# Kernel tuning notes

Measured on AMD Instinct MI355X. Metric: run time of the kernel, lower is better.

Reference implementation:

```python
import jax, jax.numpy as jnp
import numpy as np

E = 200      # word2vec_embed_size
D = 768      # hidden_size
LN_EPS = 1e-12


def setup_inputs() -> dict:
    key = jax.random.key(0)
    ks = jax.random.split(key, 9)
    B, L, W = 16, 512, 8
    std = 0.02
    return {
        "word_embeddings": jax.random.normal(ks[0], (B, L, W, E), jnp.float32),
        "layer_output": jax.random.normal(ks[1], (B, L, D), jnp.float32),
        "Wt": jax.random.normal(ks[2], (D, E), jnp.float32) * std,   # word_transform weight
        "bt": jnp.zeros((D,), jnp.float32),
        "Ww": jax.random.normal(ks[3], (D, D), jnp.float32) * std,   # word_word_weight weight
        "bw": jnp.zeros((D,), jnp.float32),
        "attn_W": jax.random.normal(ks[4], (D, D), jnp.float32) * std,
        "ln_gamma": jnp.ones((D,), jnp.float32),
        "ln_beta": jnp.zeros((D,), jnp.float32),
    }


def _layernorm(x, gamma, beta):
    mu = jnp.mean(x, axis=-1, keepdims=True)
    var = jnp.mean(jnp.square(x - mu), axis=-1, keepdims=True)
    return (x - mu) * jax.lax.rsqrt(var + LN_EPS) * gamma + beta


def reference(word_embeddings, layer_output, Wt, bt, Ww, bw, attn_W, ln_gamma, ln_beta):
    # word_transform -> tanh -> word_word_weight   (dropout = identity in eval)
    wo = jnp.tanh(jnp.einsum('blwe,de->blwd', word_embeddings, Wt) + bt)
    wo = jnp.einsum('blwd,ed->blwe', wo, Ww) + bw          # [B,L,W,D]
    # bilinear char-word attention: (layer @ attn_W) . wo over D
    q = jnp.einsum('bld,de->ble', layer_output, attn_W)    # [B,L,D]
    alpha = jnp.einsum('bld,blwd->blw', q, wo)             # [B,L,W]
    alpha = jax.nn.softmax(alpha, axis=-1)
    weighted = jnp.einsum('blw,blwd->bld', alpha, wo)      # [B,L,D]
    fused = layer_output + weighted                        # residual (dropout = identity)
    return _layernorm(fused, ln_gamma, ln_beta)
```

## Files before the change

### kernel.cpp

```cpp
#include <hip/hip_runtime.h>
#include <hip/hip_bf16.h>


typedef __bf16 bf16_t;
typedef bf16_t bf16x4 __attribute__((ext_vector_type(4)));
typedef bf16_t bf16x8 __attribute__((ext_vector_type(8)));
typedef float f32x4 __attribute__((ext_vector_type(4)));

__device__ __forceinline__ bf16x4 cvt4(float4 v) {
  bf16x4 o;
  o[0] = (bf16_t)v.x; o[1] = (bf16_t)v.y;
  o[2] = (bf16_t)v.z; o[3] = (bf16_t)v.w;
  return o;
}
__device__ __forceinline__ bf16x8 cvt8(float4 a, float4 b) {
  bf16x8 v;
  v[0] = (bf16_t)a.x; v[1] = (bf16_t)a.y; v[2] = (bf16_t)a.z; v[3] = (bf16_t)a.w;
  v[4] = (bf16_t)b.x; v[5] = (bf16_t)b.y; v[6] = (bf16_t)b.z; v[7] = (bf16_t)b.w;
  return v;
}

__global__ void prep_all(const float* __restrict__ LO,
                         const float* __restrict__ Wt,
                         const float* __restrict__ Ww,
                         bf16_t* __restrict__ LOb, bf16_t* __restrict__ Wtb,
                         bf16_t* __restrict__ Wwf) {
  const int bid = blockIdx.x;
  if (bid >= 372) {
    const long u = (long)(bid - 372) * 256 + threadIdx.x;
    float4 a = *(const float4*)(LO + u * 8);
    float4 b = *(const float4*)(LO + u * 8 + 4);
    *(bf16x8*)&LOb[u * 8] = cvt8(a, b);
  } else if (bid < 84) {
    const int u = bid * 256 + threadIdx.x;
    const int lane = u & 63;
    const int v = u >> 6;
    const int kt = v % 7;
    const int v2 = v / 7;
    const int jg = v2 & 7, nt = v2 >> 3;
    const int l16 = lane & 15, quad = lane >> 4;
    const int n = nt * 128 + jg * 16 + l16;
    const int k0 = kt * 32 + quad * 8;
    float4 a = {0.f, 0.f, 0.f, 0.f}, b = {0.f, 0.f, 0.f, 0.f};
    if (k0 < 200) {
      a = *(const float4*)(Wt + n * 200 + k0);
      b = *(const float4*)(Wt + n * 200 + k0 + 4);
    }
    *(bf16x4*)&Wtb[u * 8] = cvt4(a);
    *(bf16x4*)&Wtb[u * 8 + 4] = cvt4(b);
  } else {
    const int u = (bid - 84) * 256 + threadIdx.x;
    const int lane = u & 63;
    const int v = u >> 6;
    const int kt = v % 24;
    const int jg = v / 24;
    const int l16 = lane & 15, quad = lane >> 4;
    const long n = jg * 16 + l16;
    const int k0 = kt * 32 + quad * 8;
    float4 a = *(const float4*)(Ww + n * 768 + k0);
    float4 b = *(const float4*)(Ww + n * 768 + k0 + 4);
    *(bf16x4*)&Wwf[u * 8] = cvt4(a);
    *(bf16x4*)&Wwf[u * 8 + 4] = cvt4(b);
  }
}

__global__ void prep_wc(const float* __restrict__ Wc, bf16_t* __restrict__ Wcf) {
  const int u = blockIdx.x * 256 + threadIdx.x;
  const int lane = u & 63;
  const int v = u >> 6;
  const int kt = v % 24;
  const int jg = v / 24;
  const int l16 = lane & 15, quad = lane >> 4;
  const int n = jg * 16 + l16;
  const int k0 = kt * 32 + quad * 8;
  bf16x8 o;
#pragma unroll
  for (int e = 0; e < 8; ++e) o[e] = (bf16_t)Wc[(long)(k0 + e) * 768 + n];
  *(bf16x8*)&Wcf[u * 8] = o;
}

__global__ __launch_bounds__(256, 2) void gemm_nn64(
    const float* __restrict__ A, const float* __restrict__ B,
    float* __restrict__ C) {
  __shared__ __align__(16) bf16_t As[64 * 32];
  __shared__ __align__(16) bf16_t Bs[32 * 64];

  const int t = threadIdx.x;
  const int lane = t & 63, wave = t >> 6;
  const int wr = wave >> 1, wc = wave & 1;
  const int quad = lane >> 4, l16 = lane & 15;
  const int m0 = blockIdx.y * 64, n0 = blockIdx.x * 64;

  f32x4 acc[2][2] = {};

  for (int kt = 0; kt < 24; ++kt) {
    const int k0 = kt * 32;
#pragma unroll
    for (int r = 0; r < 2; ++r) {
      const int f = r * 256 + t;
      const int arow = f >> 3, ak = (f & 7) * 4;
      *(bf16x4*)&As[arow * 32 + ak] =
          cvt4(*(const float4*)(A + (m0 + arow) * 768 + k0 + ak));
      const int brow = f >> 4, bc = (f & 15) * 4;
      *(bf16x4*)&Bs[brow * 64 + bc] =
          cvt4(*(const float4*)(B + (long)(k0 + brow) * 768 + n0 + bc));
    }
    __syncthreads();
    bf16x8 af[2], bfv[2];
#pragma unroll
    for (int i = 0; i < 2; ++i)
      af[i] = *(const bf16x8*)&As[(wr * 32 + i * 16 + l16) * 32 + quad * 8];
#pragma unroll
    for (int j = 0; j < 2; ++j) {
      const int n = wc * 32 + j * 16 + l16;
#pragma unroll
      for (int jj = 0; jj < 8; ++jj)
        bfv[j][jj] = Bs[(quad * 8 + jj) * 64 + n];
    }
#pragma unroll
    for (int i = 0; i < 2; ++i)
#pragma unroll
      for (int j = 0; j < 2; ++j)
        acc[i][j] = __builtin_amdgcn_mfma_f32_16x16x32_bf16(af[i], bfv[j],
                                                            acc[i][j], 0, 0, 0);
    __syncthreads();
  }

#pragma unroll
  for (int j = 0; j < 2; ++j) {
    const int n = n0 + wc * 32 + j * 16 + l16;
#pragma unroll
    for (int i = 0; i < 2; ++i) {
      const int mBase = m0 + wr * 32 + i * 16 + quad * 4;
#pragma unroll
      for (int r = 0; r < 4; ++r)
        C[(long)(mBase + r) * 768 + n] = acc[i][j][r];
    }
  }
}

__global__ __launch_bounds__(1024) void gemm_r(
    const bf16_t* __restrict__ LOb, const bf16_t* __restrict__ Wcf,
    float* __restrict__ Rout) {
  const int t = threadIdx.x;
  const int lane = t & 63, w = t >> 6;
  const int quad = lane >> 4, l16 = lane & 15;
  const long m0 = (long)blockIdx.x * 32;

  const bf16_t* a0p = LOb + (m0 + l16) * 768 + quad * 8;
  const bf16_t* a1p = LOb + (m0 + 16 + l16) * 768 + quad * 8;
  const bf16_t* bp = Wcf + ((size_t)(w * 3) * 24 << 9) + lane * 8;

  f32x4 acc[2][3] = {};
  bf16x8 afC[2], afP[2], bfC[3], bfP[3];

#define LDA_R(dst, kt_)                                             \
  {                                                                 \
    dst[0] = *(const bf16x8*)(a0p + (kt_) * 32);                    \
    dst[1] = *(const bf16x8*)(a1p + (kt_) * 32);                    \
  }
#define LDB_R(dst, kt_)                                             \
  {                                                                 \
    _Pragma("unroll") for (int j_ = 0; j_ < 3; ++j_)                \
        dst[j_] = *(const bf16x8*)(bp + ((j_ * 24 + (kt_)) << 9));  \
  }

  LDA_R(afC, 0); LDB_R(bfC, 0);
#pragma unroll
  for (int kt = 0; kt < 24; ++kt) {
    if (kt < 23) { LDA_R(afP, kt + 1); LDB_R(bfP, kt + 1); }
#pragma unroll
    for (int i = 0; i < 2; ++i)
#pragma unroll
      for (int j = 0; j < 3; ++j)
        acc[i][j] = __builtin_amdgcn_mfma_f32_16x16x32_bf16(afC[i], bfC[j],
                                                            acc[i][j], 0, 0, 0);
    if (kt < 23) {
#pragma unroll
      for (int i = 0; i < 2; ++i) afC[i] = afP[i];
#pragma unroll
      for (int j = 0; j < 3; ++j) bfC[j] = bfP[j];
    }
  }
#undef LDA_R
#undef LDB_R

#pragma unroll
  for (int i = 0; i < 2; ++i)
#pragma unroll
    for (int j = 0; j < 3; ++j) {
      const int n = w * 48 + j * 16 + l16;
#pragma unroll
      for (int r = 0; r < 4; ++r) {
        const int ml = i * 16 + quad * 4 + r;
        Rout[(m0 + ml) * 768 + n] = acc[i][j][r];
      }
    }
}

#define ASF_LD 232
__global__ __launch_bounds__(256, 2) void x1_attn(
    const float* __restrict__ WE, const bf16_t* __restrict__ Wtb,
    const float* __restrict__ bt, const float* __restrict__ R,
    bf16_t* __restrict__ Yb) {
  __shared__ __align__(16) bf16_t As[32 * ASF_LD];
  __shared__ __align__(16) bf16_t Ybuf[4 * 768];
  __shared__ float red[4][8][4];
  __shared__ float alphaS[4][8];

  const int t = threadIdx.x;
  const int lane = t & 63, wc = t >> 6;
  const int quad = lane >> 4, l16 = lane & 15;
  const int ghalf = quad >> 1, wq = (quad & 1) * 4;
  const long m0 = (long)blockIdx.x * 32;
  const long gbase = (long)blockIdx.x * 4;

  const float* WEb = WE + m0 * 200;
#pragma unroll
  for (int r = 0; r < 7; ++r) {
    const int f = r * 256 + t;
    if (f < 1600) {
      const int row = f / 50, idx = f - row * 50;
      *(bf16x4*)&As[row * ASF_LD + idx * 4] =
          cvt4(*(const float4*)(WEb + 4 * f));
    }
  }
  {
    const bf16x4 z4 = {(bf16_t)0.f, (bf16_t)0.f, (bf16_t)0.f, (bf16_t)0.f};
    *(bf16x4*)&As[(t >> 3) * ASF_LD + 200 + (t & 7) * 4] = z4;
  }
  __syncthreads();

  bf16x4 st[6][2][2];
  float pl[2][4] = {};

  const bf16_t* bbase = Wtb + (size_t)lane * 8;

  bf16x8 bfC0 = *(const bf16x8*)(bbase + (size_t)(((wc * 2 + 0) * 7) << 9));
  bf16x8 bfC1 = *(const bf16x8*)(bbase + (size_t)(((wc * 2 + 1) * 7) << 9));
  bf16x8 bfP0, bfP1;

#pragma unroll
  for (int nt = 0; nt < 6; ++nt) {
    f32x4 acc[2][2] = {};
#pragma unroll
    for (int kt = 0; kt < 7; ++kt) {
      if (!(nt == 5 && kt == 6)) {
        const int nnt = (kt == 6) ? nt + 1 : nt;
        const int nkt = (kt == 6) ? 0 : kt + 1;
        bfP0 = *(const bf16x8*)(bbase +
                                (size_t)(((nnt * 8 + wc * 2 + 0) * 7 + nkt) << 9));
        bfP1 = *(const bf16x8*)(bbase +
                                (size_t)(((nnt * 8 + wc * 2 + 1) * 7 + nkt) << 9));
      }
      bf16x8 af0 = *(const bf16x8*)&As[l16 * ASF_LD + kt * 32 + quad * 8];
      bf16x8 af1 = *(const bf16x8*)&As[(16 + l16) * ASF_LD + kt * 32 + quad * 8];
      acc[0][0] = __builtin_amdgcn_mfma_f32_16x16x32_bf16(af0, bfC0, acc[0][0], 0, 0, 0);
      acc[0][1] = __builtin_amdgcn_mfma_f32_16x16x32_bf16(af0, bfC1, acc[0][1], 0, 0, 0);
      acc[1][0] = __builtin_amdgcn_mfma_f32_16x16x32_bf16(af1, bfC0, acc[1][0], 0, 0, 0);
      acc[1][1] = __builtin_amdgcn_mfma_f32_16x16x32_bf16(af1, bfC1, acc[1][1], 0, 0, 0);
      bfC0 = bfP0; bfC1 = bfP1;
    }
    const int nb = nt * 128 + wc * 32;
#pragma unroll
    for (int j = 0; j < 2; ++j) {
      const int n = nb + j * 16 + l16;
      const float btv = bt[n];
#pragma unroll
      for (int i = 0; i < 2; ++i) {
        const float Rv = R[(gbase + i * 2 + ghalf) * 768 + n];
#pragma unroll
        for (int r = 0; r < 4; ++r) {
          const float vv = acc[i][j][r] + btv;
          const float e = __expf(2.f * vv);
          const float x = 1.f - __fdividef(2.f, e + 1.f);
          st[nt][i][j][r] = (bf16_t)x;
          pl[i][r] += x * Rv;
        }
      }
    }
  }

#pragma unroll
  for (int o = 8; o > 0; o >>= 1)
#pragma unroll
    for (int i = 0; i < 2; ++i)
#pragma unroll
      for (int r = 0; r < 4; ++r)
        pl[i][r] += __shfl_down(pl[i][r], o, 16);
  if (l16 == 0)
#pragma unroll
    for (int i = 0; i < 2; ++i)
#pragma unroll
      for (int r = 0; r < 4; ++r)
        red[i * 2 + ghalf][wq + r][wc] = pl[i][r];
  __syncthreads();

  if (t < 32) {
    const int g = t >> 3, w8 = t & 7;
    const float lg = red[g][w8][0] + red[g][w8][1] + red[g][w8][2] + red[g][w8][3];
    float mx = lg;
#pragma unroll
    for (int o = 4; o > 0; o >>= 1) mx = fmaxf(mx, __shfl_xor(mx, o, 8));
    const float e = __expf(lg - mx);
    float s = e;
#pragma unroll
    for (int o = 4; o > 0; o >>= 1) s += __shfl_xor(s, o, 8);
    alphaS[g][w8] = __fdividef(e, s);
  }
  __syncthreads();

#pragma unroll
  for (int i = 0; i < 2; ++i) {
    const int glo = i * 2 + ghalf;
    const float a0 = alphaS[glo][wq + 0], a1 = alphaS[glo][wq + 1];
    const float a2 = alphaS[glo][wq + 2], a3 = alphaS[glo][wq + 3];
#pragma unroll
    for (int nt = 0; nt < 6; ++nt)
#pragma unroll
      for (int j = 0; j < 2; ++j) {
        float py = a0 * (float)st[nt][i][j][0] + a1 * (float)st[nt][i][j][1] +
                   a2 * (float)st[nt][i][j][2] + a3 * (float)st[nt][i][j][3];
        py += __shfl_xor(py, 16);
        if ((quad & 1) == 0)
          Ybuf[glo * 768 + nt * 128 + wc * 32 + j * 16 + l16] = (bf16_t)py;
      }
  }
  __syncthreads();
  {
    const float4* src = (const float4*)Ybuf;
    float4* dst = (float4*)(Yb + gbase * 768);
    dst[t] = src[t];
    if (t < 128) dst[256 + t] = src[256 + t];
  }
}

__global__ __launch_bounds__(1024) void y_ww_ln(
    const bf16_t* __restrict__ Yb, const bf16_t* __restrict__ Wwf,
    const float* __restrict__ bw, const float* __restrict__ LO,
    const float* __restrict__ gamma, const float* __restrict__ beta,
    float* __restrict__ out) {
  __shared__ float rowstats[16][32][2];
  __shared__ float mustd[32][2];

  const int t = threadIdx.x;
  const int lane = t & 63, w = t >> 6;
  const int quad = lane >> 4, l16 = lane & 15;
  const long m0 = (long)blockIdx.x * 32;

  const bf16_t* a0p = Yb + (m0 + l16) * 768 + quad * 8;
  const bf16_t* a1p = Yb + (m0 + 16 + l16) * 768 + quad * 8;
  const bf16_t* bp = Wwf + ((size_t)(w * 3) * 24 << 9) + lane * 8;

  f32x4 acc[2][3] = {};
  bf16x8 afC[2], afP[2], bfC[3], bfP[3];

#define LDA_Y(dst, kt_)                                             \
  {                                                                 \
    dst[0] = *(const bf16x8*)(a0p + (kt_) * 32);                    \
    dst[1] = *(const bf16x8*)(a1p + (kt_) * 32);                    \
  }
#define LDB_Y(dst, kt_)                                             \
  {                                                                 \
    _Pragma("unroll") for (int j_ = 0; j_ < 3; ++j_)                \
        dst[j_] = *(const bf16x8*)(bp + ((j_ * 24 + (kt_)) << 9));  \
  }

  LDA_Y(afC, 0); LDB_Y(bfC, 0);
#pragma unroll
  for (int kt = 0; kt < 24; ++kt) {
    if (kt < 23) { LDA_Y(afP, kt + 1); LDB_Y(bfP, kt + 1); }
#pragma unroll
    for (int i = 0; i < 2; ++i)
#pragma unroll
      for (int j = 0; j < 3; ++j)
        acc[i][j] = __builtin_amdgcn_mfma_f32_16x16x32_bf16(afC[i], bfC[j],
                                                            acc[i][j], 0, 0, 0);
    if (kt < 23) {
#pragma unroll
      for (int i = 0; i < 2; ++i) afC[i] = afP[i];
#pragma unroll
      for (int j = 0; j < 3; ++j) bfC[j] = bfP[j];
    }
  }
#undef LDA_Y
#undef LDB_Y

  float s1[2][4] = {}, s2[2][4] = {};
#pragma unroll
  for (int i = 0; i < 2; ++i)
#pragma unroll
    for (int j = 0; j < 3; ++j) {
      const int n = w * 48 + j * 16 + l16;
      const float bwv = bw[n];
#pragma unroll
      for (int r = 0; r < 4; ++r) {
        const int ml = i * 16 + quad * 4 + r;
        const float fv = acc[i][j][r] + bwv + LO[(m0 + ml) * 768 + n];
        acc[i][j][r] = fv;
        s1[i][r] += fv;
        s2[i][r] += fv * fv;
      }
    }
#pragma unroll
  for (int o = 8; o > 0; o >>= 1)
#pragma unroll
    for (int i = 0; i < 2; ++i)
#pragma unroll
      for (int r = 0; r < 4; ++r) {
        s1[i][r] += __shfl_down(s1[i][r], o, 16);
        s2[i][r] += __shfl_down(s2[i][r], o, 16);
      }
  if (l16 == 0)
#pragma unroll
    for (int i = 0; i < 2; ++i)
#pragma unroll
      for (int r = 0; r < 4; ++r) {
        const int ml = i * 16 + quad * 4 + r;
        rowstats[w][ml][0] = s1[i][r];
        rowstats[w][ml][1] = s2[i][r];
      }
  __syncthreads();

  if (t < 32) {
    float S1 = 0.f, S2 = 0.f;
#pragma unroll
    for (int ww = 0; ww < 16; ++ww) {
      S1 += rowstats[ww][t][0];
      S2 += rowstats[ww][t][1];
    }
    const float mu = S1 * (1.f / 768.f);
    const float var = S2 * (1.f / 768.f) - mu * mu;
    mustd[t][0] = mu;
    mustd[t][1] = rsqrtf(var + 1e-12f);
  }
  __syncthreads();

#pragma unroll
  for (int i = 0; i < 2; ++i)
#pragma unroll
    for (int j = 0; j < 3; ++j) {
      const int n = w * 48 + j * 16 + l16;
      const float gv = gamma[n], bv = beta[n];
#pragma unroll
      for (int r = 0; r < 4; ++r) {
        const int ml = i * 16 + quad * 4 + r;
        out[(m0 + ml) * 768 + n] =
            (acc[i][j][r] - mustd[ml][0]) * mustd[ml][1] * gv + bv;
      }
    }
}

extern "C" void kernel_launch(void* const* d_in, const int* in_sizes, int n_in,
                              void* d_out, int out_size, void* d_ws,
                              size_t ws_size, hipStream_t stream) {
  (void)in_sizes; (void)n_in; (void)out_size; (void)ws_size;
  const float* WE = (const float*)d_in[0];
  const float* LO = (const float*)d_in[1];
  const float* Wt = (const float*)d_in[2];
  const float* bt = (const float*)d_in[3];
  const float* Ww = (const float*)d_in[4];
  const float* bw = (const float*)d_in[5];
  const float* aW = (const float*)d_in[6];
  const float* g  = (const float*)d_in[7];
  const float* bb = (const float*)d_in[8];
  float* out = (float*)d_out;

  char* ws = (char*)d_ws;
  const size_t WC_BYTES  = (size_t)768 * 768 * 4;
  const size_t WTB_BYTES = (size_t)6 * 8 * 7 * 64 * 8 * 2;
  const size_t WWF_BYTES = (size_t)48 * 24 * 64 * 8 * 2;
  const size_t WCF_BYTES = WWF_BYTES;
  float*  Wc  = (float*)ws;
  bf16_t* Wtb = (bf16_t*)(ws + WC_BYTES);
  bf16_t* Wwf = (bf16_t*)(ws + WC_BYTES + WTB_BYTES);
  bf16_t* Wcf = (bf16_t*)(ws + WC_BYTES + WTB_BYTES + WWF_BYTES);
  bf16_t* Yb  = (bf16_t*)(ws + WC_BYTES + WTB_BYTES + WWF_BYTES + WCF_BYTES);
  bf16_t* LOb = Yb;

  const dim3 blk(256);
  const dim3 blk1k(1024);

  prep_all<<<dim3(3444), blk, 0, stream>>>(LO, Wt, Ww, LOb, Wtb, Wwf);
  gemm_nn64<<<dim3(12, 12), blk, 0, stream>>>(aW, Ww, Wc);
  prep_wc<<<dim3(288), blk, 0, stream>>>(Wc, Wcf);
  gemm_r<<<dim3(256), blk1k, 0, stream>>>(LOb, Wcf, out);
  x1_attn<<<dim3(2048), blk, 0, stream>>>(WE, Wtb, bt, out, Yb);
  y_ww_ln<<<dim3(256), blk1k, 0, stream>>>(Yb, Wwf, bw, LO, g, bb, out);
}
```

Baseline: 268.4 us.

## Fuse weight-product GEMM with fragment repacking and widen attention kernel to 8 waves

```diff
diff --git a/kernel.cpp b/kernel.cpp
--- a/kernel.cpp
+++ b/kernel.cpp
@@ -24,10 +24,10 @@
                          const float* __restrict__ Wt,
                          const float* __restrict__ Ww,
                          bf16_t* __restrict__ LOb, bf16_t* __restrict__ Wtb,
-                         bf16_t* __restrict__ Wwf) {
+                         bf16_t* __restrict__ Wwf, bf16_t* __restrict__ Wwn) {
   const int bid = blockIdx.x;
-  if (bid >= 372) {
-    const long u = (long)(bid - 372) * 256 + threadIdx.x;
+  if (bid >= 660) {
+    const long u = (long)(bid - 660) * 256 + threadIdx.x;
     float4 a = *(const float4*)(LO + u * 8);
     float4 b = *(const float4*)(LO + u * 8 + 4);
     *(bf16x8*)&LOb[u * 8] = cvt8(a, b);
@@ -48,7 +48,7 @@
     }
     *(bf16x4*)&Wtb[u * 8] = cvt4(a);
     *(bf16x4*)&Wtb[u * 8 + 4] = cvt4(b);
-  } else {
+  } else if (bid < 372) {
     const int u = (bid - 84) * 256 + threadIdx.x;
     const int lane = u & 63;
     const int v = u >> 6;
@@ -61,81 +61,92 @@
     float4 b = *(const float4*)(Ww + n * 768 + k0 + 4);
     *(bf16x4*)&Wwf[u * 8] = cvt4(a);
     *(bf16x4*)&Wwf[u * 8 + 4] = cvt4(b);
-  }
-}
-
-__global__ void prep_wc(const float* __restrict__ Wc, bf16_t* __restrict__ Wcf) {
-  const int u = blockIdx.x * 256 + threadIdx.x;
-  const int lane = u & 63;
-  const int v = u >> 6;
-  const int kt = v % 24;
-  const int jg = v / 24;
-  const int l16 = lane & 15, quad = lane >> 4;
-  const int n = jg * 16 + l16;
-  const int k0 = kt * 32 + quad * 8;
-  bf16x8 o;
-#pragma unroll
-  for (int e = 0; e < 8; ++e) o[e] = (bf16_t)Wc[(long)(k0 + e) * 768 + n];
-  *(bf16x8*)&Wcf[u * 8] = o;
-}
-
-__global__ __launch_bounds__(256, 2) void gemm_nn64(
-    const float* __restrict__ A, const float* __restrict__ B,
-    float* __restrict__ C) {
-  __shared__ __align__(16) bf16_t As[64 * 32];
-  __shared__ __align__(16) bf16_t Bs[32 * 64];
+  } else {
+    const int u = (bid - 372) * 256 + threadIdx.x;
+    const int lane = u & 63;
+    const int v = u >> 6;
+    const int kt = v % 24;
+    const int jg = v / 24;
+    const int l16 = lane & 15, quad = lane >> 4;
+    const int n = jg * 16 + l16;
+    const int k0 = kt * 32 + quad * 8;
+    bf16x8 o;
+#pragma unroll
+    for (int e = 0; e < 8; ++e) o[e] = (bf16_t)Ww[(long)(k0 + e) * 768 + n];
+    *(bf16x8*)&Wwn[u * 8] = o;
+  }
+}
+
+__global__ __launch_bounds__(1024) void gemm_wc(
+    const float* __restrict__ aW, const bf16_t* __restrict__ Wwn,
+    bf16_t* __restrict__ Wcf) {
+  __shared__ bf16_t Cs[32][768];
 
   const int t = threadIdx.x;
-  const int lane = t & 63, wave = t >> 6;
-  const int wr = wave >> 1, wc = wave & 1;
+  const int lane = t & 63, w = t >> 6;
   const int quad = lane >> 4, l16 = lane & 15;
-  const int m0 = blockIdx.y * 64, n0 = blockIdx.x * 64;
-
-  f32x4 acc[2][2] = {};
-
+  const int m0 = blockIdx.x * 32;
+
+  const float* a0p = aW + (long)(m0 + l16) * 768 + quad * 8;
+  const float* a1p = aW + (long)(m0 + 16 + l16) * 768 + quad * 8;
+  const bf16_t* bp = Wwn + ((size_t)(w * 3) * 24 << 9) + lane * 8;
+
+  f32x4 acc[2][3] = {};
+  bf16x8 afC[2], afP[2], bfC[3], bfP[3];
+
+#define LDA_W(dst, kt_)                                              \
+  {                                                                  \
+    dst[0] = cvt8(*(const float4*)(a0p + (kt_) * 32),                \
+                  *(const float4*)(a0p + (kt_) * 32 + 4));           \
+    dst[1] = cvt8(*(const float4*)(a1p + (kt_) * 32),                \
+                  *(const float4*)(a1p + (kt_) * 32 + 4));           \
+  }
+#define LDB_W(dst, kt_)                                              \
+  {                                                                  \
+    _Pragma("unroll") for (int j_ = 0; j_ < 3; ++j_)                 \
+        dst[j_] = *(const bf16x8*)(bp + ((j_ * 24 + (kt_)) << 9));   \
+  }
+
+  LDA_W(afC, 0); LDB_W(bfC, 0);
+#pragma unroll
   for (int kt = 0; kt < 24; ++kt) {
-    const int k0 = kt * 32;
-#pragma unroll
-    for (int r = 0; r < 2; ++r) {
-      const int f = r * 256 + t;
-      const int arow = f >> 3, ak = (f & 7) * 4;
-      *(bf16x4*)&As[arow * 32 + ak] =
-          cvt4(*(const float4*)(A + (m0 + arow) * 768 + k0 + ak));
-      const int brow = f >> 4, bc = (f & 15) * 4;
-      *(bf16x4*)&Bs[brow * 64 + bc] =
-          cvt4(*(const float4*)(B + (long)(k0 + brow) * 768 + n0 + bc));
-    }
-    __syncthreads();
-    bf16x8 af[2], bfv[2];
-#pragma unroll
-    for (int i = 0; i < 2; ++i)
-      af[i] = *(const bf16x8*)&As[(wr * 32 + i * 16 + l16) * 32 + quad * 8];
-#pragma unroll
-    for (int j = 0; j < 2; ++j) {
-      const int n = wc * 32 + j * 16 + l16;
-#pragma unroll
-      for (int jj = 0; jj < 8; ++jj)
-        bfv[j][jj] = Bs[(quad * 8 + jj) * 64 + n];
-    }
-#pragma unroll
-    for (int i = 0; i < 2; ++i)
-#pragma unroll
-      for (int j = 0; j < 2; ++j)
-        acc[i][j] = __builtin_amdgcn_mfma_f32_16x16x32_bf16(af[i], bfv[j],
+    if (kt < 23) { LDA_W(afP, kt + 1); LDB_W(bfP, kt + 1); }
+#pragma unroll
+    for (int i = 0; i < 2; ++i)
+#pragma unroll
+      for (int j = 0; j < 3; ++j)
+        acc[i][j] = __builtin_amdgcn_mfma_f32_16x16x32_bf16(afC[i], bfC[j],
                                                             acc[i][j], 0, 0, 0);
-    __syncthreads();
-  }
-
-#pragma unroll
-  for (int j = 0; j < 2; ++j) {
-    const int n = n0 + wc * 32 + j * 16 + l16;
-#pragma unroll
-    for (int i = 0; i < 2; ++i) {
-      const int mBase = m0 + wr * 32 + i * 16 + quad * 4;
+    if (kt < 23) {
+#pragma unroll
+      for (int i = 0; i < 2; ++i) afC[i] = afP[i];
+#pragma unroll
+      for (int j = 0; j < 3; ++j) bfC[j] = bfP[j];
+    }
+  }
+#undef LDA_W
+#undef LDB_W
+
+#pragma unroll
+  for (int i = 0; i < 2; ++i)
+#pragma unroll
+    for (int j = 0; j < 3; ++j) {
+      const int n = w * 48 + j * 16 + l16;
 #pragma unroll
       for (int r = 0; r < 4; ++r)
-        C[(long)(mBase + r) * 768 + n] = acc[i][j][r];
-    }
+        Cs[i * 16 + quad * 4 + r][n] = (bf16_t)acc[i][j][r];
+    }
+  __syncthreads();
+
+#pragma unroll
+  for (int c0 = 0; c0 < 3; ++c0) {
+    const int c = c0 * 1024 + t;
+    const int jg = c >> 6, lane2 = c & 63;
+    const int q2 = lane2 >> 4, s16 = lane2 & 15;
+    bf16x8 o;
+#pragma unroll
+    for (int e = 0; e < 8; ++e) o[e] = Cs[q2 * 8 + e][jg * 16 + s16];
+    *(bf16x8*)&Wcf[((size_t)(jg * 24 + blockIdx.x) * 64 + lane2) * 8] = o;
   }
 }
 
@@ -199,86 +210,83 @@
 }
 
 #define ASF_LD 232
-__global__ __launch_bounds__(256, 2) void x1_attn(
+__global__ __launch_bounds__(512, 2) void x1_attn(
     const float* __restrict__ WE, const bf16_t* __restrict__ Wtb,
     const float* __restrict__ bt, const float* __restrict__ R,
     bf16_t* __restrict__ Yb) {
   __shared__ __align__(16) bf16_t As[32 * ASF_LD];
   __shared__ __align__(16) bf16_t Ybuf[4 * 768];
-  __shared__ float red[4][8][4];
+  __shared__ float red[4][8][8];
   __shared__ float alphaS[4][8];
 
   const int t = threadIdx.x;
-  const int lane = t & 63, wc = t >> 6;
+  const int lane = t & 63, w = t >> 6;
   const int quad = lane >> 4, l16 = lane & 15;
   const int ghalf = quad >> 1, wq = (quad & 1) * 4;
   const long m0 = (long)blockIdx.x * 32;
   const long gbase = (long)blockIdx.x * 4;
 
+  float rv[2][6], bt6[6];
+#pragma unroll
+  for (int nt = 0; nt < 6; ++nt) {
+    const int n = nt * 128 + w * 16 + l16;
+    bt6[nt] = bt[n];
+#pragma unroll
+    for (int i = 0; i < 2; ++i)
+      rv[i][nt] = R[(gbase + i * 2 + ghalf) * 768 + n];
+  }
+
   const float* WEb = WE + m0 * 200;
 #pragma unroll
-  for (int r = 0; r < 7; ++r) {
-    const int f = r * 256 + t;
+  for (int r = 0; r < 4; ++r) {
+    const int f = r * 512 + t;
     if (f < 1600) {
       const int row = f / 50, idx = f - row * 50;
       *(bf16x4*)&As[row * ASF_LD + idx * 4] =
           cvt4(*(const float4*)(WEb + 4 * f));
     }
   }
-  {
+  if (t < 256) {
     const bf16x4 z4 = {(bf16_t)0.f, (bf16_t)0.f, (bf16_t)0.f, (bf16_t)0.f};
     *(bf16x4*)&As[(t >> 3) * ASF_LD + 200 + (t & 7) * 4] = z4;
   }
   __syncthreads();
 
-  bf16x4 st[6][2][2];
+  bf16x4 st[6][2];
   float pl[2][4] = {};
 
   const bf16_t* bbase = Wtb + (size_t)lane * 8;
 
-  bf16x8 bfC0 = *(const bf16x8*)(bbase + (size_t)(((wc * 2 + 0) * 7) << 9));
-  bf16x8 bfC1 = *(const bf16x8*)(bbase + (size_t)(((wc * 2 + 1) * 7) << 9));
-  bf16x8 bfP0, bfP1;
+  bf16x8 bfC = *(const bf16x8*)(bbase + ((size_t)(w * 7) << 9));
+  bf16x8 bfP;
 
 #pragma unroll
   for (int nt = 0; nt < 6; ++nt) {
-    f32x4 acc[2][2] = {};
+    f32x4 acc[2] = {};
 #pragma unroll
     for (int kt = 0; kt < 7; ++kt) {
       if (!(nt == 5 && kt == 6)) {
         const int nnt = (kt == 6) ? nt + 1 : nt;
         const int nkt = (kt == 6) ? 0 : kt + 1;
-        bfP0 = *(const bf16x8*)(bbase +
-                                (size_t)(((nnt * 8 + wc * 2 + 0) * 7 + nkt) << 9));
-        bfP1 = *(const bf16x8*)(bbase +
-                                (size_t)(((nnt * 8 + wc * 2 + 1) * 7 + nkt) << 9));
+        bfP = *(const bf16x8*)(bbase +
+                               ((size_t)((nnt * 8 + w) * 7 + nkt) << 9));
       }
       bf16x8 af0 = *(const bf16x8*)&As[l16 * ASF_LD + kt * 32 + quad * 8];
       bf16x8 af1 = *(const bf16x8*)&As[(16 + l16) * ASF_LD + kt * 32 + quad * 8];
-      acc[0][0] = __builtin_amdgcn_mfma_f32_16x16x32_bf16(af0, bfC0, acc[0][0], 0, 0, 0);
-      acc[0][1] = __builtin_amdgcn_mfma_f32_16x16x32_bf16(af0, bfC1, acc[0][1], 0, 0, 0);
-      acc[1][0] = __builtin_amdgcn_mfma_f32_16x16x32_bf16(af1, bfC0, acc[1][0], 0, 0, 0);
-      acc[1][1] = __builtin_amdgcn_mfma_f32_16x16x32_bf16(af1, bfC1, acc[1][1], 0, 0, 0);
-      bfC0 = bfP0; bfC1 = bfP1;
-    }
-    const int nb = nt * 128 + wc * 32;
-#pragma unroll
-    for (int j = 0; j < 2; ++j) {
-      const int n = nb + j * 16 + l16;
-      const float btv = bt[n];
-#pragma unroll
-      for (int i = 0; i < 2; ++i) {
-        const float Rv = R[(gbase + i * 2 + ghalf) * 768 + n];
-#pragma unroll
-        for (int r = 0; r < 4; ++r) {
-          const float vv = acc[i][j][r] + btv;
-          const float e = __expf(2.f * vv);
-          const float x = 1.f - __fdividef(2.f, e + 1.f);
-          st[nt][i][j][r] = (bf16_t)x;
-          pl[i][r] += x * Rv;
-        }
-      }
-    }
+      acc[0] = __builtin_amdgcn_mfma_f32_16x16x32_bf16(af0, bfC, acc[0], 0, 0, 0);
+      acc[1] = __builtin_amdgcn_mfma_f32_16x16x32_bf16(af1, bfC, acc[1], 0, 0, 0);
+      bfC = bfP;
+    }
+#pragma unroll
+    for (int i = 0; i < 2; ++i)
+#pragma unroll
+      for (int r = 0; r < 4; ++r) {
+        const float vv = acc[i][r] + bt6[nt];
+        const float e = __expf(2.f * vv);
+        const float x = 1.f - __fdividef(2.f, e + 1.f);
+        st[nt][i][r] = (bf16_t)x;
+        pl[i][r] += x * rv[i][nt];
+      }
   }
 
 #pragma unroll
@@ -293,12 +301,14 @@
     for (int i = 0; i < 2; ++i)
 #pragma unroll
       for (int r = 0; r < 4; ++r)
-        red[i * 2 + ghalf][wq + r][wc] = pl[i][r];
+        red[i * 2 + ghalf][wq + r][w] = pl[i][r];
   __syncthreads();
 
   if (t < 32) {
     const int g = t >> 3, w8 = t & 7;
-    const float lg = red[g][w8][0] + red[g][w8][1] + red[g][w8][2] + red[g][w8][3];
+    float lg = 0.f;
+#pragma unroll
+    for (int v = 0; v < 8; ++v) lg += red[g][w8][v];
     float mx = lg;
 #pragma unroll
     for (int o = 4; o > 0; o >>= 1) mx = fmaxf(mx, __shfl_xor(mx, o, 8));
@@ -316,22 +326,19 @@
     const float a0 = alphaS[glo][wq + 0], a1 = alphaS[glo][wq + 1];
     const float a2 = alphaS[glo][wq + 2], a3 = alphaS[glo][wq + 3];
 #pragma unroll
-    for (int nt = 0; nt < 6; ++nt)
-#pragma unroll
-      for (int j = 0; j < 2; ++j) {
-        float py = a0 * (float)st[nt][i][j][0] + a1 * (float)st[nt][i][j][1] +
-                   a2 * (float)st[nt][i][j][2] + a3 * (float)st[nt][i][j][3];
-        py += __shfl_xor(py, 16);
-        if ((quad & 1) == 0)
-          Ybuf[glo * 768 + nt * 128 + wc * 32 + j * 16 + l16] = (bf16_t)py;
-      }
-  }
-  __syncthreads();
-  {
+    for (int nt = 0; nt < 6; ++nt) {
+      float py = a0 * (float)st[nt][i][0] + a1 * (float)st[nt][i][1] +
+                 a2 * (float)st[nt][i][2] + a3 * (float)st[nt][i][3];
+      py += __shfl_xor(py, 16);
+      if ((quad & 1) == 0)
+        Ybuf[glo * 768 + nt * 128 + w * 16 + l16] = (bf16_t)py;
+    }
+  }
+  __syncthreads();
+  if (t < 384) {
     const float4* src = (const float4*)Ybuf;
     float4* dst = (float4*)(Yb + gbase * 768);
     dst[t] = src[t];
-    if (t < 128) dst[256 + t] = src[256 + t];
   }
 }
 
@@ -467,24 +474,21 @@
   float* out = (float*)d_out;
 
   char* ws = (char*)d_ws;
-  const size_t WC_BYTES  = (size_t)768 * 768 * 4;
   const size_t WTB_BYTES = (size_t)6 * 8 * 7 * 64 * 8 * 2;
   const size_t WWF_BYTES = (size_t)48 * 24 * 64 * 8 * 2;
-  const size_t WCF_BYTES = WWF_BYTES;
-  float*  Wc  = (float*)ws;
-  bf16_t* Wtb = (bf16_t*)(ws + WC_BYTES);
-  bf16_t* Wwf = (bf16_t*)(ws + WC_BYTES + WTB_BYTES);
-  bf16_t* Wcf = (bf16_t*)(ws + WC_BYTES + WTB_BYTES + WWF_BYTES);
-  bf16_t* Yb  = (bf16_t*)(ws + WC_BYTES + WTB_BYTES + WWF_BYTES + WCF_BYTES);
+  bf16_t* Wtb = (bf16_t*)ws;
+  bf16_t* Wwf = (bf16_t*)(ws + WTB_BYTES);
+  bf16_t* Wwn = (bf16_t*)(ws + WTB_BYTES + WWF_BYTES);
+  bf16_t* Wcf = (bf16_t*)(ws + WTB_BYTES + 2 * WWF_BYTES);
+  bf16_t* Yb  = (bf16_t*)(ws + WTB_BYTES + 3 * WWF_BYTES);
   bf16_t* LOb = Yb;
 
   const dim3 blk(256);
   const dim3 blk1k(1024);
 
-  prep_all<<<dim3(3444), blk, 0, stream>>>(LO, Wt, Ww, LOb, Wtb, Wwf);
-  gemm_nn64<<<dim3(12, 12), blk, 0, stream>>>(aW, Ww, Wc);
-  prep_wc<<<dim3(288), blk, 0, stream>>>(Wc, Wcf);
+  prep_all<<<dim3(3732), blk, 0, stream>>>(LO, Wt, Ww, LOb, Wtb, Wwf, Wwn);
+  gemm_wc<<<dim3(24), blk1k, 0, stream>>>(aW, Wwn, Wcf);
   gemm_r<<<dim3(256), blk1k, 0, stream>>>(LOb, Wcf, out);
-  x1_attn<<<dim3(2048), blk, 0, stream>>>(WE, Wtb, bt, out, Yb);
+  x1_attn<<<dim3(2048), dim3(512), 0, stream>>>(WE, Wtb, bt, out, Yb);
   y_ww_ln<<<dim3(256), blk1k, 0, stream>>>(Yb, Wwf, bw, LO, g, bb, out);
 }
```

New measurement: 327.2 us. 21.9% more time.

## Reorder Wt prepacking per jg and deepen B-fragment prefetch to three stages

Applied to the files above, without the earlier changes.

```diff
diff --git a/kernel.cpp b/kernel.cpp
--- a/kernel.cpp
+++ b/kernel.cpp
@@ -36,8 +36,9 @@
     const int lane = u & 63;
     const int v = u >> 6;
     const int kt = v % 7;
-    const int v2 = v / 7;
-    const int jg = v2 & 7, nt = v2 >> 3;
+    const int r2 = v / 7;
+    const int nt = r2 % 6;
+    const int jg = r2 / 6;
     const int l16 = lane & 15, quad = lane >> 4;
     const int n = nt * 128 + jg * 16 + l16;
     const int k0 = kt * 32 + quad * 8;
@@ -215,6 +216,16 @@
   const long m0 = (long)blockIdx.x * 32;
   const long gbase = (long)blockIdx.x * 4;
 
+  const bf16_t* bb0 = Wtb + (((size_t)(wc * 2 + 0) * 42) << 9) + (size_t)lane * 8;
+  const bf16_t* bb1 = Wtb + (((size_t)(wc * 2 + 1) * 42) << 9) + (size_t)lane * 8;
+
+  bf16x8 S[3][2];
+#pragma unroll
+  for (int p = 0; p < 3; ++p) {
+    S[p][0] = *(const bf16x8*)(bb0 + ((size_t)p << 9));
+    S[p][1] = *(const bf16x8*)(bb1 + ((size_t)p << 9));
+  }
+
   const float* WEb = WE + m0 * 200;
 #pragma unroll
   for (int r = 0; r < 7; ++r) {
@@ -234,32 +245,23 @@
   bf16x4 st[6][2][2];
   float pl[2][4] = {};
 
-  const bf16_t* bbase = Wtb + (size_t)lane * 8;
-
-  bf16x8 bfC0 = *(const bf16x8*)(bbase + (size_t)(((wc * 2 + 0) * 7) << 9));
-  bf16x8 bfC1 = *(const bf16x8*)(bbase + (size_t)(((wc * 2 + 1) * 7) << 9));
-  bf16x8 bfP0, bfP1;
-
 #pragma unroll
   for (int nt = 0; nt < 6; ++nt) {
     f32x4 acc[2][2] = {};
 #pragma unroll
     for (int kt = 0; kt < 7; ++kt) {
-      if (!(nt == 5 && kt == 6)) {
-        const int nnt = (kt == 6) ? nt + 1 : nt;
-        const int nkt = (kt == 6) ? 0 : kt + 1;
-        bfP0 = *(const bf16x8*)(bbase +
-                                (size_t)(((nnt * 8 + wc * 2 + 0) * 7 + nkt) << 9));
-        bfP1 = *(const bf16x8*)(bbase +
-                                (size_t)(((nnt * 8 + wc * 2 + 1) * 7 + nkt) << 9));
-      }
+      const int u = nt * 7 + kt;
+      const int s = u % 3;
       bf16x8 af0 = *(const bf16x8*)&As[l16 * ASF_LD + kt * 32 + quad * 8];
       bf16x8 af1 = *(const bf16x8*)&As[(16 + l16) * ASF_LD + kt * 32 + quad * 8];
-      acc[0][0] = __builtin_amdgcn_mfma_f32_16x16x32_bf16(af0, bfC0, acc[0][0], 0, 0, 0);
-      acc[0][1] = __builtin_amdgcn_mfma_f32_16x16x32_bf16(af0, bfC1, acc[0][1], 0, 0, 0);
-      acc[1][0] = __builtin_amdgcn_mfma_f32_16x16x32_bf16(af1, bfC0, acc[1][0], 0, 0, 0);
-      acc[1][1] = __builtin_amdgcn_mfma_f32_16x16x32_bf16(af1, bfC1, acc[1][1], 0, 0, 0);
-      bfC0 = bfP0; bfC1 = bfP1;
+      acc[0][0] = __builtin_amdgcn_mfma_f32_16x16x32_bf16(af0, S[s][0], acc[0][0], 0, 0, 0);
+      acc[0][1] = __builtin_amdgcn_mfma_f32_16x16x32_bf16(af0, S[s][1], acc[0][1], 0, 0, 0);
+      acc[1][0] = __builtin_amdgcn_mfma_f32_16x16x32_bf16(af1, S[s][0], acc[1][0], 0, 0, 0);
+      acc[1][1] = __builtin_amdgcn_mfma_f32_16x16x32_bf16(af1, S[s][1], acc[1][1], 0, 0, 0);
+      if (u + 3 < 42) {
+        S[s][0] = *(const bf16x8*)(bb0 + ((size_t)(u + 3) << 9));
+        S[s][1] = *(const bf16x8*)(bb1 + ((size_t)(u + 3) << 9));
+      }
     }
     const int nb = nt * 128 + wc * 32;
 #pragma unroll
```

After: 283.5 us. +5.6%, slower.
